# Optimization experiments

Hardware: AMD Instinct MI355X
Metric: run time of the kernel (lower is better)

## Reference

```python
import jax, jax.numpy as jnp
import numpy as np

N_QUBITS = 10
Q_DEPTH = 6


def _apply_1q(state, gate, wire):
    """Apply a 2x2 gate (or batched [B,2,2] gates) to `wire` of state [B,2,...,2]."""
    s = jnp.moveaxis(state, wire + 1, -1)
    if gate.ndim == 2:
        s = s @ gate.T  # new_j = sum_i G[j,i] * old_i
    else:
        s = jnp.einsum('b...i,bji->b...j', s, gate)
    return jnp.moveaxis(s, -1, wire + 1)


def _apply_cnot(state, ctrl, tgt):
    s = jnp.moveaxis(state, (ctrl + 1, tgt + 1), (-2, -1))
    s = jnp.stack([s[..., 0, :], s[..., 1, ::-1]], axis=-2)  # flip target where ctrl=1
    return jnp.moveaxis(s, (-2, -1), (ctrl + 1, tgt + 1))


def _ry(theta):
    """RY(theta) = [[cos(t/2), -sin(t/2)], [sin(t/2), cos(t/2)]]; theta scalar or [B]."""
    c, s = jnp.cos(theta / 2.0), jnp.sin(theta / 2.0)
    return jnp.stack([jnp.stack([c, -s], -1), jnp.stack([s, c], -1)], -2)


def _vqc(angles, q_weights):
    """angles: [B, n_qubits] per-sample RY angles; q_weights: [q_depth, n_qubits].
    Returns <PauliZ_w> for every wire: [B, n_qubits]. All gates are real -> float32 state."""
    B, n = angles.shape
    q_depth = q_weights.shape[0]
    # H-layer on |0...0> gives the uniform superposition: all amplitudes 2^{-n/2}
    state = jnp.full((B,) + (2,) * n, 2.0 ** (-n / 2.0), dtype=angles.dtype)
    # RY layer with per-sample input angles
    for w in range(n):
        state = _apply_1q(state, _ry(angles[:, w]), w)
    # q_depth x (brick-wall CNOT entangler + trainable RY layer)
    for k in range(q_depth):
        for i in range(0, n - 1, 2):
            state = _apply_cnot(state, i, i + 1)
        for i in range(1, n - 1, 2):
            state = _apply_cnot(state, i, i + 1)
        for w in range(n):
            state = _apply_1q(state, _ry(q_weights[k, w]), w)
    # expval(PauliZ(w)) = P(wire w = 0) - P(wire w = 1)
    probs = state * state  # real statevector
    exps = []
    for w in range(n):
        p = jnp.moveaxis(probs, w + 1, 1).reshape(B, 2, -1).sum(-1)
        exps.append(p[:, 0] - p[:, 1])
    return jnp.stack(exps, -1)


def setup_inputs() -> dict:
    key = jax.random.key(0)
    ks = jax.random.split(key, 6)
    B, D_IN, OUT = 8192, 512, 64
    x = jax.random.normal(ks[0], (B, D_IN), dtype=jnp.float32)
    W1 = jax.random.normal(ks[1], (D_IN, N_QUBITS), dtype=jnp.float32) * (1.0 / np.sqrt(D_IN))
    b1 = jnp.zeros((N_QUBITS,), dtype=jnp.float32)
    # keras 'uniform' initializer: U(-0.05, 0.05)
    q_weights = jax.random.uniform(ks[2], (Q_DEPTH, N_QUBITS), dtype=jnp.float32,
                                   minval=-0.05, maxval=0.05)
    W2 = jax.random.normal(ks[3], (N_QUBITS, OUT), dtype=jnp.float32) * (1.0 / np.sqrt(N_QUBITS))
    b2 = jnp.zeros((OUT,), dtype=jnp.float32)
    return {"x": x, "W1": W1, "b1": b1, "q_weights": q_weights, "W2": W2, "b2": b2}


def reference(x, W1, b1, q_weights, W2, b2):
    # Dense(n_qubits, tanh) then scale to angles in (-pi/2, pi/2)
    angles = jnp.tanh(x @ W1 + b1) * (jnp.pi / 2.0)  # [B, n_qubits]
    q_out = _vqc(angles, q_weights)                   # [B, n_qubits]
    return q_out @ W2 + b2                            # [B, output_dim]
```

## Files before the change

kernel.cpp:

```cpp
#include <hip/hip_runtime.h>

#define NQ 10
#define QD 6
#define DIN 512
#define DOUT 64

typedef float v2f __attribute__((ext_vector_type(2)));

__device__ __forceinline__ v2f sp(float s) { v2f r; r.x = s; r.y = s; return r; }
__device__ __forceinline__ v2f mk(float a, float b) { v2f r; r.x = a; r.y = b; return r; }
#define PKF(a, b, c) __builtin_elementwise_fma(a, b, c)

template <int CTRL>
__device__ __forceinline__ float dppf(float v) {
    return __int_as_float(__builtin_amdgcn_mov_dpp(__float_as_int(v), CTRL, 0xF, 0xF, true));
}
template <int M>
__device__ __forceinline__ float sx(float v) {
    if constexpr (M == 1)      return dppf<0xB1>(v);
    else if constexpr (M == 2) return dppf<0x4E>(v);
    else if constexpr (M == 4) return dppf<0x1B>(dppf<0x141>(v));
    else                       return dppf<0x128>(v);
}
template <int M>
__device__ __forceinline__ v2f sx2(v2f v) { return mk(sx<M>(v.x), sx<M>(v.y)); }
__device__ __forceinline__ float red16(float v) {
    v += dppf<0x128>(v);
    v += dppf<0x124>(v);
    v += dppf<0x122>(v);
    v += dppf<0x121>(v);
    return v;
}

__global__ __launch_bounds__(256, 2) void dqc_main(
    const float* __restrict__ x,
    const float* __restrict__ W1,
    const float* __restrict__ b1,
    const float* __restrict__ qw,
    const float* __restrict__ W2,
    const float* __restrict__ b2,
    float* __restrict__ out,
    const int B)
{
    __shared__ __align__(16) float csl[2 * QD * NQ];

    const int tid = threadIdx.x;
    if (tid < QD * NQ) {
        float s, c;
        sincosf(qw[tid] * 0.5f, &s, &c);
        csl[2 * tid] = c; csl[2 * tid + 1] = s;
    }

    const int lane16 = tid & 15;
    const int b  = (blockIdx.x * 256 + tid) >> 4;
    const int bb = (b < B) ? b : (B - 1);

    float xr[32];
    {
        const float4* xp = (const float4*)(x + (size_t)bb * DIN + lane16 * 32);
        #pragma unroll
        for (int i = 0; i < 8; ++i) {
            const float4 v = xp[i];
            xr[4*i] = v.x; xr[4*i+1] = v.y; xr[4*i+2] = v.z; xr[4*i+3] = v.w;
        }
    }
    float dot[NQ];
    #pragma unroll
    for (int w = 0; w < NQ; ++w) dot[w] = 0.f;
    {
        const float4* wp = (const float4*)(W1 + (size_t)lane16 * 32 * NQ);
        #pragma unroll
        for (int j = 0; j < 16; ++j) {
            const float4 f0 = wp[5*j], f1 = wp[5*j+1], f2 = wp[5*j+2],
                         f3 = wp[5*j+3], f4 = wp[5*j+4];
            const float xa = xr[2*j], xb = xr[2*j+1];
            dot[0]=fmaf(xa,f0.x,dot[0]); dot[1]=fmaf(xa,f0.y,dot[1]);
            dot[2]=fmaf(xa,f0.z,dot[2]); dot[3]=fmaf(xa,f0.w,dot[3]);
            dot[4]=fmaf(xa,f1.x,dot[4]); dot[5]=fmaf(xa,f1.y,dot[5]);
            dot[6]=fmaf(xa,f1.z,dot[6]); dot[7]=fmaf(xa,f1.w,dot[7]);
            dot[8]=fmaf(xa,f2.x,dot[8]); dot[9]=fmaf(xa,f2.y,dot[9]);
            dot[0]=fmaf(xb,f2.z,dot[0]); dot[1]=fmaf(xb,f2.w,dot[1]);
            dot[2]=fmaf(xb,f3.x,dot[2]); dot[3]=fmaf(xb,f3.y,dot[3]);
            dot[4]=fmaf(xb,f3.z,dot[4]); dot[5]=fmaf(xb,f3.w,dot[5]);
            dot[6]=fmaf(xb,f4.x,dot[6]); dot[7]=fmaf(xb,f4.y,dot[7]);
            dot[8]=fmaf(xb,f4.z,dot[8]); dot[9]=fmaf(xb,f4.w,dot[9]);
        }
    }
    #pragma unroll
    for (int w = 0; w < NQ; ++w) dot[w] = red16(dot[w]);

    float u0[NQ], u1[NQ];
    #pragma unroll
    for (int w = 0; w < NQ; ++w) {
        const float th2 = tanhf(dot[w] + b1[w]) * 0.78539816339744830962f;
        float s, c;
        sincosf(th2, &s, &c);
        const float isq2 = 0.70710678118654752440f;
        u0[w] = (c - s) * isq2;
        u1[w] = (c + s) * isq2;
    }

    v2f A[32];
    {
        float lf = ((lane16 & 8) ? u1[0] : u0[0]);
        lf *= ((((lane16 >> 2) ^ (lane16 >> 3)) & 1) ? u1[1] : u0[1]);
        lf *= ((lane16 & 2) ? u1[2] : u0[2]);
        lf *= (((lane16 ^ (lane16 >> 1)) & 1) ? u1[3] : u0[3]);
        #pragma unroll
        for (int m = 0; m < 32; ++m) {
            float f = ((m & 16) ? u1[4] : u0[4]);
            f *= ((((m >> 3) ^ (m >> 4)) & 1) ? u1[5] : u0[5]);
            f *= ((m & 4) ? u1[6] : u0[6]);
            f *= ((((m >> 1) ^ (m >> 2)) & 1) ? u1[7] : u0[7]);
            f *= ((m & 1) ? u1[8] : u0[8]);
            f *= lf;
            A[m] = (m & 1) ? mk(f * u1[9], f * u0[9]) : mk(f * u0[9], f * u1[9]);
        }
    }

    __syncthreads();

    #pragma unroll 1
    for (int k = 0; k < QD; ++k) {
        const float4* cp = (const float4*)(csl + k * 2 * NQ);
        const float4 g0 = cp[0], g1 = cp[1], g2 = cp[2], g3 = cp[3], g4 = cp[4];
        const float C0=g0.x,S0=g0.y, C1=g0.z,S1=g0.w;
        const float C2=g1.x,S2=g1.y, C3=g1.z,S3=g1.w;
        const float C4=g2.x,S4=g2.y, C5=g2.z,S5=g2.w;
        const float C6=g3.x,S6=g3.y, C7=g3.z,S7=g3.w;
        const float C8=g4.x,S8=g4.y, C9=g4.z,S9=g4.w;
        const bool fuse = (k < QD - 1);

        {
            const float g = (lane16 & 8) ? S0 : -S0;
            const v2f al = sp(C0), be = sp(g);
            #pragma unroll
            for (int m = 0; m < 32; ++m) { const v2f p = sx2<8>(A[m]); A[m] = PKF(al, A[m], be * p); }
        }
        {
            const float g = (lane16 & 2) ? S2 : -S2;
            const bool cb = (lane16 & 4) != 0;
            const v2f al = sp(cb ? g : C2), be = sp(cb ? C2 : g);
            #pragma unroll
            for (int m = 0; m < 32; ++m) { const v2f p = sx2<2>(A[m]); A[m] = PKF(al, A[m], be * p); }
        }
        {
            const bool cb = (lane16 & 1) != 0;
            const v2f a0 = sp(cb ? -S4 : C4), b0 = sp(cb ? C4 : -S4);
            const v2f a1 = sp(cb ?  S4 : C4), b1v = sp(cb ? C4 :  S4);
            #pragma unroll
            for (int m = 0; m < 16; ++m) {
                const v2f lo = A[m], hi = A[m + 16];
                A[m]      = PKF(a0, lo, b0 * hi);
                A[m + 16] = PKF(a1, hi, b1v * lo);
            }
        }
        {
            #pragma unroll
            for (int m = 0; m < 32; ++m) {
                if (m & 4) continue;
                const v2f lo = A[m], hi = A[m + 4];
                if ((m >> 3) & 1) {
                    A[m]     = PKF(sp(-S6), lo, sp(C6) * hi);
                    A[m + 4] = PKF(sp( S6), hi, sp(C6) * lo);
                } else {
                    A[m]     = PKF(sp(C6), lo, sp(-S6) * hi);
                    A[m + 4] = PKF(sp(C6), hi, sp( S6) * lo);
                }
            }
        }
        {
            #pragma unroll
            for (int q = 0; q < 16; ++q) {
                const v2f lo = A[2*q], hi = A[2*q+1];
                if (q & 1) {
                    A[2*q]   = PKF(sp(-S8), lo, sp(C8) * hi);
                    A[2*q+1] = PKF(sp( S8), hi, sp(C8) * lo);
                } else {
                    A[2*q]   = PKF(sp(C8), lo, sp(-S8) * hi);
                    A[2*q+1] = PKF(sp(C8), hi, sp( S8) * lo);
                }
            }
        }

        {
            const float g = (lane16 & 4) ? S1 : -S1;
            const bool cb = fuse && ((lane16 & 8) != 0);
            const v2f al = sp(cb ? -g : C1), be = sp(cb ? C1 : g);
            #pragma unroll
            for (int m = 0; m < 32; ++m) { const v2f p = sx2<4>(A[m]); A[m] = PKF(al, A[m], be * p); }
        }
        {
            const float g = (lane16 & 1) ? S3 : -S3;
            const bool cb = fuse && ((lane16 & 2) != 0);
            const v2f al = sp(cb ? -g : C3), be = sp(cb ? C3 : g);
            #pragma unroll
            for (int m = 0; m < 32; ++m) { const v2f p = sx2<1>(A[m]); A[m] = PKF(al, A[m], be * p); }
        }
        {
            const float a0c = fuse ?  S5 : C5,  b0c = fuse ? C5 : -S5;
            const float a1c = fuse ? -S5 : C5,  b1c = fuse ? C5 :  S5;
            #pragma unroll
            for (int m = 0; m < 32; ++m) {
                if (m & 8) continue;
                const v2f lo = A[m], hi = A[m + 8];
                if ((m >> 4) & 1) {
                    A[m]     = PKF(sp(a0c), lo, sp(b0c) * hi);
                    A[m + 8] = PKF(sp(a1c), hi, sp(b1c) * lo);
                } else {
                    A[m]     = PKF(sp(C5), lo, sp(-S5) * hi);
                    A[m + 8] = PKF(sp(C5), hi, sp( S5) * lo);
                }
            }
        }
        {
            const float a0c = fuse ?  S7 : C7,  b0c = fuse ? C7 : -S7;
            const float a1c = fuse ? -S7 : C7,  b1c = fuse ? C7 :  S7;
            #pragma unroll
            for (int m = 0; m < 32; ++m) {
                if (m & 2) continue;
                const v2f lo = A[m], hi = A[m + 2];
                if ((m >> 2) & 1) {
                    A[m]     = PKF(sp(a0c), lo, sp(b0c) * hi);
                    A[m + 2] = PKF(sp(a1c), hi, sp(b1c) * lo);
                } else {
                    A[m]     = PKF(sp(C7), lo, sp(-S7) * hi);
                    A[m + 2] = PKF(sp(C7), hi, sp( S7) * lo);
                }
            }
        }
        {
            const v2f Ae = sp(C9), Be = mk(-S9, S9);
            const v2f Ao = fuse ? mk(S9, -S9) : Ae;
            const v2f Bo = fuse ? sp(C9) : Be;
            #pragma unroll
            for (int m = 0; m < 32; ++m) {
                const v2f s = mk(A[m].y, A[m].x);
                A[m] = (m & 1) ? PKF(Ao, A[m], Bo * s) : PKF(Ae, A[m], Be * s);
            }
        }
    }

    v2f tot2 = sp(0.f), q4 = sp(0.f), q5 = sp(0.f), q6 = sp(0.f), q7 = sp(0.f), q8 = sp(0.f);
    #pragma unroll
    for (int m = 0; m < 32; ++m) {
        const v2f P = A[m] * A[m];
        tot2 += P;
        if (m & 16) q4 += P;
        if (m & 8)  q5 += P;
        if (m & 4)  q6 += P;
        if (m & 2)  q7 += P;
        if (m & 1)  q8 += P;
    }
    const float tot = tot2.x + tot2.y;
    float e[NQ];
    e[0] = (lane16 & 8) ? -tot : tot;
    e[1] = (lane16 & 4) ? -tot : tot;
    e[2] = (lane16 & 2) ? -tot : tot;
    e[3] = (lane16 & 1) ? -tot : tot;
    e[4] = tot - 2.f * (q4.x + q4.y);
    e[5] = tot - 2.f * (q5.x + q5.y);
    e[6] = tot - 2.f * (q6.x + q6.y);
    e[7] = tot - 2.f * (q7.x + q7.y);
    e[8] = tot - 2.f * (q8.x + q8.y);
    e[9] = tot - 2.f * tot2.y;
    #pragma unroll
    for (int w = 0; w < NQ; ++w) e[w] = red16(e[w]);

    if (b < B) {
        float4 o = ((const float4*)b2)[lane16];
        #pragma unroll
        for (int w = 0; w < NQ; ++w) {
            const float4 wv = ((const float4*)(W2 + w * DOUT))[lane16];
            o.x = fmaf(e[w], wv.x, o.x);
            o.y = fmaf(e[w], wv.y, o.y);
            o.z = fmaf(e[w], wv.z, o.z);
            o.w = fmaf(e[w], wv.w, o.w);
        }
        ((float4*)(out + (size_t)b * DOUT))[lane16] = o;
    }
}

extern "C" void kernel_launch(void* const* d_in, const int* in_sizes, int n_in,
                              void* d_out, int out_size, void* d_ws, size_t ws_size,
                              hipStream_t stream) {
    const float* x  = (const float*)d_in[0];
    const float* W1 = (const float*)d_in[1];
    const float* b1 = (const float*)d_in[2];
    const float* qw = (const float*)d_in[3];
    const float* W2 = (const float*)d_in[4];
    const float* b2 = (const float*)d_in[5];
    float* out = (float*)d_out;

    const int B = in_sizes[0] / DIN;
    const int blocks = (B + 15) / 16;
    dqc_main<<<blocks, 256, 0, stream>>>(x, W1, b1, qw, W2, b2, out, B);
}
```

Before: 111.6 us.

## Spread each sample's statevector over 32 lanes instead of 16

Each sample's 1024-amplitude statevector is now split across 32 lanes holding 32 amplitudes each, down from 16 lanes holding 64. Qubit 4 moves from a register index to a lane index, and a ds_swizzle handles the 16-lane exchange. The change halves the registers per thread, raises launch_bounds occupancy from 2 to 4, and doubles the thread count per sample. The cost is more cross-lane shuffles, including a slower ds_swizzle per gate on qubit 0, and a longer reduction.

```diff
diff --git a/kernel.cpp b/kernel.cpp
--- a/kernel.cpp
+++ b/kernel.cpp
@@ -17,22 +17,24 @@
 }
 template <int M>
 __device__ __forceinline__ float sx(float v) {
-    if constexpr (M == 1)      return dppf<0xB1>(v);
-    else if constexpr (M == 2) return dppf<0x4E>(v);
-    else if constexpr (M == 4) return dppf<0x1B>(dppf<0x141>(v));
-    else                       return dppf<0x128>(v);
+    if constexpr (M == 1)       return dppf<0xB1>(v);
+    else if constexpr (M == 2)  return dppf<0x4E>(v);
+    else if constexpr (M == 4)  return dppf<0x1B>(dppf<0x141>(v));
+    else if constexpr (M == 8)  return dppf<0x128>(v);
+    else return __int_as_float(__builtin_amdgcn_ds_swizzle(__float_as_int(v), 0x401F));
 }
 template <int M>
 __device__ __forceinline__ v2f sx2(v2f v) { return mk(sx<M>(v.x), sx<M>(v.y)); }
-__device__ __forceinline__ float red16(float v) {
+__device__ __forceinline__ float red32(float v) {
     v += dppf<0x128>(v);
     v += dppf<0x124>(v);
     v += dppf<0x122>(v);
     v += dppf<0x121>(v);
+    v += sx<16>(v);
     return v;
 }
 
-__global__ __launch_bounds__(256, 2) void dqc_main(
+__global__ __launch_bounds__(256, 4) void dqc_main(
     const float* __restrict__ x,
     const float* __restrict__ W1,
     const float* __restrict__ b1,
@@ -51,15 +53,15 @@
         csl[2 * tid] = c; csl[2 * tid + 1] = s;
     }
 
-    const int lane16 = tid & 15;
-    const int b  = (blockIdx.x * 256 + tid) >> 4;
+    const int lane32 = tid & 31;
+    const int b  = (blockIdx.x * 256 + tid) >> 5;
     const int bb = (b < B) ? b : (B - 1);
 
-    float xr[32];
+    float xr[16];
     {
-        const float4* xp = (const float4*)(x + (size_t)bb * DIN + lane16 * 32);
-        #pragma unroll
-        for (int i = 0; i < 8; ++i) {
+        const float4* xp = (const float4*)(x + (size_t)bb * DIN + lane32 * 16);
+        #pragma unroll
+        for (int i = 0; i < 4; ++i) {
             const float4 v = xp[i];
             xr[4*i] = v.x; xr[4*i+1] = v.y; xr[4*i+2] = v.z; xr[4*i+3] = v.w;
         }
@@ -68,9 +70,9 @@
     #pragma unroll
     for (int w = 0; w < NQ; ++w) dot[w] = 0.f;
     {
-        const float4* wp = (const float4*)(W1 + (size_t)lane16 * 32 * NQ);
-        #pragma unroll
-        for (int j = 0; j < 16; ++j) {
+        const float4* wp = (const float4*)(W1 + (size_t)lane32 * 16 * NQ);
+        #pragma unroll
+        for (int j = 0; j < 8; ++j) {
             const float4 f0 = wp[5*j], f1 = wp[5*j+1], f2 = wp[5*j+2],
                          f3 = wp[5*j+3], f4 = wp[5*j+4];
             const float xa = xr[2*j], xb = xr[2*j+1];
@@ -87,7 +89,7 @@
         }
     }
     #pragma unroll
-    for (int w = 0; w < NQ; ++w) dot[w] = red16(dot[w]);
+    for (int w = 0; w < NQ; ++w) dot[w] = red32(dot[w]);
 
     float u0[NQ], u1[NQ];
     #pragma unroll
@@ -100,16 +102,19 @@
         u1[w] = (c + s) * isq2;
     }
 
-    v2f A[32];
+    v2f A[16];
     {
-        float lf = ((lane16 & 8) ? u1[0] : u0[0]);
-        lf *= ((((lane16 >> 2) ^ (lane16 >> 3)) & 1) ? u1[1] : u0[1]);
-        lf *= ((lane16 & 2) ? u1[2] : u0[2]);
-        lf *= (((lane16 ^ (lane16 >> 1)) & 1) ? u1[3] : u0[3]);
-        #pragma unroll
-        for (int m = 0; m < 32; ++m) {
-            float f = ((m & 16) ? u1[4] : u0[4]);
-            f *= ((((m >> 3) ^ (m >> 4)) & 1) ? u1[5] : u0[5]);
+        float lf = ((lane32 & 16) ? u1[0] : u0[0]);
+        lf *= ((((lane32 >> 3) ^ (lane32 >> 4)) & 1) ? u1[1] : u0[1]);
+        lf *= ((lane32 & 4) ? u1[2] : u0[2]);
+        lf *= ((((lane32 >> 1) ^ (lane32 >> 2)) & 1) ? u1[3] : u0[3]);
+        lf *= ((lane32 & 1) ? u1[4] : u0[4]);
+        const bool b0 = (lane32 & 1) != 0;
+        const float w5a = b0 ? u1[5] : u0[5];
+        const float w5b = b0 ? u0[5] : u1[5];
+        #pragma unroll
+        for (int m = 0; m < 16; ++m) {
+            float f = ((m & 8) ? w5b : w5a);
             f *= ((m & 4) ? u1[6] : u0[6]);
             f *= ((((m >> 1) ^ (m >> 2)) & 1) ? u1[7] : u0[7]);
             f *= ((m & 1) ? u1[8] : u0[8]);
@@ -132,32 +137,28 @@
         const bool fuse = (k < QD - 1);
 
         {
-            const float g = (lane16 & 8) ? S0 : -S0;
+            const float g = (lane32 & 16) ? S0 : -S0;
             const v2f al = sp(C0), be = sp(g);
             #pragma unroll
-            for (int m = 0; m < 32; ++m) { const v2f p = sx2<8>(A[m]); A[m] = PKF(al, A[m], be * p); }
-        }
-        {
-            const float g = (lane16 & 2) ? S2 : -S2;
-            const bool cb = (lane16 & 4) != 0;
+            for (int m = 0; m < 16; ++m) { const v2f p = sx2<16>(A[m]); A[m] = PKF(al, A[m], be * p); }
+        }
+        {
+            const float g = (lane32 & 4) ? S2 : -S2;
+            const bool cb = (lane32 & 8) != 0;
             const v2f al = sp(cb ? g : C2), be = sp(cb ? C2 : g);
             #pragma unroll
-            for (int m = 0; m < 32; ++m) { const v2f p = sx2<2>(A[m]); A[m] = PKF(al, A[m], be * p); }
-        }
-        {
-            const bool cb = (lane16 & 1) != 0;
-            const v2f a0 = sp(cb ? -S4 : C4), b0 = sp(cb ? C4 : -S4);
-            const v2f a1 = sp(cb ?  S4 : C4), b1v = sp(cb ? C4 :  S4);
+            for (int m = 0; m < 16; ++m) { const v2f p = sx2<4>(A[m]); A[m] = PKF(al, A[m], be * p); }
+        }
+        {
+            const float g = (lane32 & 1) ? S4 : -S4;
+            const bool cb = (lane32 & 2) != 0;
+            const v2f al = sp(cb ? g : C4), be = sp(cb ? C4 : g);
+            #pragma unroll
+            for (int m = 0; m < 16; ++m) { const v2f p = sx2<1>(A[m]); A[m] = PKF(al, A[m], be * p); }
+        }
+        {
             #pragma unroll
             for (int m = 0; m < 16; ++m) {
-                const v2f lo = A[m], hi = A[m + 16];
-                A[m]      = PKF(a0, lo, b0 * hi);
-                A[m + 16] = PKF(a1, hi, b1v * lo);
-            }
-        }
-        {
-            #pragma unroll
-            for (int m = 0; m < 32; ++m) {
                 if (m & 4) continue;
                 const v2f lo = A[m], hi = A[m + 4];
                 if ((m >> 3) & 1) {
@@ -171,58 +172,51 @@
         }
         {
             #pragma unroll
-            for (int q = 0; q < 16; ++q) {
-                const v2f lo = A[2*q], hi = A[2*q+1];
-                if (q & 1) {
-                    A[2*q]   = PKF(sp(-S8), lo, sp(C8) * hi);
-                    A[2*q+1] = PKF(sp( S8), hi, sp(C8) * lo);
+            for (int m = 0; m < 16; m += 2) {
+                const v2f lo = A[m], hi = A[m + 1];
+                if ((m >> 1) & 1) {
+                    A[m]     = PKF(sp(-S8), lo, sp(C8) * hi);
+                    A[m + 1] = PKF(sp( S8), hi, sp(C8) * lo);
                 } else {
-                    A[2*q]   = PKF(sp(C8), lo, sp(-S8) * hi);
-                    A[2*q+1] = PKF(sp(C8), hi, sp( S8) * lo);
+                    A[m]     = PKF(sp(C8), lo, sp(-S8) * hi);
+                    A[m + 1] = PKF(sp(C8), hi, sp( S8) * lo);
                 }
             }
         }
 
         {
-            const float g = (lane16 & 4) ? S1 : -S1;
-            const bool cb = fuse && ((lane16 & 8) != 0);
+            const float g = (lane32 & 8) ? S1 : -S1;
+            const bool cb = fuse && ((lane32 & 16) != 0);
             const v2f al = sp(cb ? -g : C1), be = sp(cb ? C1 : g);
             #pragma unroll
-            for (int m = 0; m < 32; ++m) { const v2f p = sx2<4>(A[m]); A[m] = PKF(al, A[m], be * p); }
-        }
-        {
-            const float g = (lane16 & 1) ? S3 : -S3;
-            const bool cb = fuse && ((lane16 & 2) != 0);
+            for (int m = 0; m < 16; ++m) { const v2f p = sx2<8>(A[m]); A[m] = PKF(al, A[m], be * p); }
+        }
+        {
+            const float g = (lane32 & 2) ? S3 : -S3;
+            const bool cb = fuse && ((lane32 & 4) != 0);
             const v2f al = sp(cb ? -g : C3), be = sp(cb ? C3 : g);
             #pragma unroll
-            for (int m = 0; m < 32; ++m) { const v2f p = sx2<1>(A[m]); A[m] = PKF(al, A[m], be * p); }
-        }
-        {
-            const float a0c = fuse ?  S5 : C5,  b0c = fuse ? C5 : -S5;
-            const float a1c = fuse ? -S5 : C5,  b1c = fuse ? C5 :  S5;
-            #pragma unroll
-            for (int m = 0; m < 32; ++m) {
-                if (m & 8) continue;
+            for (int m = 0; m < 16; ++m) { const v2f p = sx2<2>(A[m]); A[m] = PKF(al, A[m], be * p); }
+        }
+        {
+            const bool cb = fuse && ((lane32 & 1) != 0);
+            const v2f a_lo = sp(cb ?  S5 : C5), b_lo = sp(cb ? C5 : -S5);
+            const v2f a_hi = sp(cb ? -S5 : C5), b_hi = sp(cb ? C5 :  S5);
+            #pragma unroll
+            for (int m = 0; m < 8; ++m) {
                 const v2f lo = A[m], hi = A[m + 8];
-                if ((m >> 4) & 1) {
-                    A[m]     = PKF(sp(a0c), lo, sp(b0c) * hi);
-                    A[m + 8] = PKF(sp(a1c), hi, sp(b1c) * lo);
-                } else {
-                    A[m]     = PKF(sp(C5), lo, sp(-S5) * hi);
-                    A[m + 8] = PKF(sp(C5), hi, sp( S5) * lo);
-                }
-            }
-        }
-        {
-            const float a0c = fuse ?  S7 : C7,  b0c = fuse ? C7 : -S7;
-            const float a1c = fuse ? -S7 : C7,  b1c = fuse ? C7 :  S7;
-            #pragma unroll
-            for (int m = 0; m < 32; ++m) {
+                A[m]     = PKF(a_lo, lo, b_lo * hi);
+                A[m + 8] = PKF(a_hi, hi, b_hi * lo);
+            }
+        }
+        {
+            #pragma unroll
+            for (int m = 0; m < 16; ++m) {
                 if (m & 2) continue;
                 const v2f lo = A[m], hi = A[m + 2];
-                if ((m >> 2) & 1) {
-                    A[m]     = PKF(sp(a0c), lo, sp(b0c) * hi);
-                    A[m + 2] = PKF(sp(a1c), hi, sp(b1c) * lo);
+                if (fuse && ((m >> 2) & 1)) {
+                    A[m]     = PKF(sp( S7), lo, sp(C7) * hi);
+                    A[m + 2] = PKF(sp(-S7), hi, sp(C7) * lo);
                 } else {
                     A[m]     = PKF(sp(C7), lo, sp(-S7) * hi);
                     A[m + 2] = PKF(sp(C7), hi, sp( S7) * lo);
@@ -234,50 +228,47 @@
             const v2f Ao = fuse ? mk(S9, -S9) : Ae;
             const v2f Bo = fuse ? sp(C9) : Be;
             #pragma unroll
-            for (int m = 0; m < 32; ++m) {
+            for (int m = 0; m < 16; ++m) {
                 const v2f s = mk(A[m].y, A[m].x);
                 A[m] = (m & 1) ? PKF(Ao, A[m], Bo * s) : PKF(Ae, A[m], Be * s);
             }
         }
     }
 
-    v2f tot2 = sp(0.f), q4 = sp(0.f), q5 = sp(0.f), q6 = sp(0.f), q7 = sp(0.f), q8 = sp(0.f);
-    #pragma unroll
-    for (int m = 0; m < 32; ++m) {
+    v2f tot2 = sp(0.f), q5 = sp(0.f), q6 = sp(0.f), q7 = sp(0.f), q8 = sp(0.f);
+    #pragma unroll
+    for (int m = 0; m < 16; ++m) {
         const v2f P = A[m] * A[m];
         tot2 += P;
-        if (m & 16) q4 += P;
-        if (m & 8)  q5 += P;
-        if (m & 4)  q6 += P;
-        if (m & 2)  q7 += P;
-        if (m & 1)  q8 += P;
+        if (m & 8) q5 += P;
+        if (m & 4) q6 += P;
+        if (m & 2) q7 += P;
+        if (m & 1) q8 += P;
     }
     const float tot = tot2.x + tot2.y;
     float e[NQ];
-    e[0] = (lane16 & 8) ? -tot : tot;
-    e[1] = (lane16 & 4) ? -tot : tot;
-    e[2] = (lane16 & 2) ? -tot : tot;
-    e[3] = (lane16 & 1) ? -tot : tot;
-    e[4] = tot - 2.f * (q4.x + q4.y);
+    e[0] = (lane32 & 16) ? -tot : tot;
+    e[1] = (lane32 & 8)  ? -tot : tot;
+    e[2] = (lane32 & 4)  ? -tot : tot;
+    e[3] = (lane32 & 2)  ? -tot : tot;
+    e[4] = (lane32 & 1)  ? -tot : tot;
     e[5] = tot - 2.f * (q5.x + q5.y);
     e[6] = tot - 2.f * (q6.x + q6.y);
     e[7] = tot - 2.f * (q7.x + q7.y);
     e[8] = tot - 2.f * (q8.x + q8.y);
     e[9] = tot - 2.f * tot2.y;
     #pragma unroll
-    for (int w = 0; w < NQ; ++w) e[w] = red16(e[w]);
+    for (int w = 0; w < NQ; ++w) e[w] = red32(e[w]);
 
     if (b < B) {
-        float4 o = ((const float4*)b2)[lane16];
+        float2 o = ((const float2*)b2)[lane32];
         #pragma unroll
         for (int w = 0; w < NQ; ++w) {
-            const float4 wv = ((const float4*)(W2 + w * DOUT))[lane16];
+            const float2 wv = ((const float2*)(W2 + w * DOUT))[lane32];
             o.x = fmaf(e[w], wv.x, o.x);
             o.y = fmaf(e[w], wv.y, o.y);
-            o.z = fmaf(e[w], wv.z, o.z);
-            o.w = fmaf(e[w], wv.w, o.w);
-        }
-        ((float4*)(out + (size_t)b * DOUT))[lane16] = o;
+        }
+        ((float2*)(out + (size_t)b * DOUT))[lane32] = o;
     }
 }
 
@@ -293,6 +284,6 @@
     float* out = (float*)d_out;
 
     const int B = in_sizes[0] / DIN;
-    const int blocks = (B + 15) / 16;
+    const int blocks = (B + 7) / 8;
     dqc_main<<<blocks, 256, 0, stream>>>(x, W1, b1, qw, W2, b2, out, B);
 }
```

Measured after the change: 108.6 us. 2.7% less time.
